# Kernel optimization log

Hardware: AMD Instinct MI355X
Metric: run time of the kernel (lower is better)

## Reference

```python
import jax, jax.numpy as jnp
import numpy as np

N_NODES = 32768   # total atoms in the batch
N_EDGES = 65536   # directed bonds (avg degree ~2)
B = 512           # graphs per batch (graphs.batch_size)
D = 64            # in_feats = hidden_feats = 64
EH = 32           # edge-MLP hidden width
N_ITERS = 6       # num_step_set2set
N_LSTM = 3        # num_layer_set2set
EPS = 1e-5


def setup_inputs() -> dict:
    key = jax.random.key(0)
    ks = iter(jax.random.split(key, 64))
    nrm = lambda shape, s: jax.random.normal(next(ks), shape, dtype=jnp.float32) * s
    inp = {
        "atom_feats": jax.random.normal(next(ks), (N_NODES, D), dtype=jnp.float32),
        "edge_feat": jax.random.uniform(next(ks), (N_EDGES, 1), dtype=jnp.float32),
        "src": jax.random.randint(next(ks), (N_EDGES,), 0, N_NODES, dtype=jnp.int32),
        "dst": jax.random.randint(next(ks), (N_EDGES,), 0, N_NODES, dtype=jnp.int32),
        "node_graph_ids": jnp.sort(jax.random.randint(next(ks), (N_NODES,), 0, B, dtype=jnp.int32)),
    }
    for l in range(2):  # two NNConv layers
        inp[f"ew1_{l}"] = nrm((EH, 1), 0.5)
        inp[f"eb1_{l}"] = nrm((EH,), 0.1)
        inp[f"ew2_{l}"] = nrm((D * D, EH), 0.05)
        inp[f"eb2_{l}"] = nrm((D * D,), 0.02)
        inp[f"cb_{l}"] = nrm((D,), 0.1)
    inp["ln_g"] = jnp.ones((D,), jnp.float32)
    inp["ln_b"] = jnp.zeros((D,), jnp.float32)
    in_sizes = [2 * D, D, D]
    for l in range(N_LSTM):
        inp[f"wih{l}"] = nrm((4 * D, in_sizes[l]), 0.1)
        inp[f"whh{l}"] = nrm((4 * D, D), 0.1)
        inp[f"bih{l}"] = nrm((4 * D,), 0.05)
        inp[f"bhh{l}"] = nrm((4 * D,), 0.05)
    inp["gn_g"] = jnp.ones((2 * D,), jnp.float32)
    inp["gn_b"] = jnp.zeros((2 * D,), jnp.float32)
    inp["fc1_w"] = nrm((2 * D, 2 * D), 0.08)
    inp["fc1_b"] = nrm((2 * D,), 0.02)
    inp["bn_g"] = jnp.ones((2 * D,), jnp.float32)
    inp["bn_b"] = jnp.zeros((2 * D,), jnp.float32)
    inp["bn_m"] = jnp.zeros((2 * D,), jnp.float32)
    inp["bn_v"] = jnp.ones((2 * D,), jnp.float32)
    inp["fc2_w"] = nrm((D, 2 * D), 0.08)
    inp["fc2_b"] = nrm((D,), 0.02)
    return inp


def _layernorm(x, g, b):
    mu = jnp.mean(x, axis=-1, keepdims=True)
    v = jnp.var(x, axis=-1, keepdims=True)
    return (x - mu) / jnp.sqrt(v + EPS) * g + b


def _nnconv(x, edge_feat, src, dst, ew1, eb1, ew2, eb2, cb):
    # edge MLP: 1 -> 32 -> D*D, reshaped to a per-edge weight matrix
    h = jax.nn.relu(edge_feat @ ew1.T + eb1)              # [E, 32]
    W = (h @ ew2.T + eb2).reshape(-1, D, D)               # [E, D, D]
    m = jnp.einsum('ei,eio->eo', x[src], W)               # per-edge matmul [E, D]
    s = jax.ops.segment_sum(m, dst, num_segments=N_NODES)
    deg = jax.ops.segment_sum(jnp.ones((m.shape[0],), m.dtype), dst, num_segments=N_NODES)
    return s / jnp.maximum(deg, 1.0)[:, None] + cb        # scatter-mean + bias


def reference(atom_feats, edge_feat, src, dst, node_graph_ids,
              ew1_0, eb1_0, ew2_0, eb2_0, cb_0,
              ew1_1, eb1_1, ew2_1, eb2_1, cb_1,
              ln_g, ln_b,
              wih0, whh0, bih0, bhh0, wih1, whh1, bih1, bhh1, wih2, whh2, bih2, bhh2,
              gn_g, gn_b, fc1_w, fc1_b, bn_g, bn_b, bn_m, bn_v, fc2_w, fc2_b):
    x = atom_feats
    for (ew1, eb1, ew2, eb2, cb) in ((ew1_0, eb1_0, ew2_0, eb2_0, cb_0),
                                     (ew1_1, eb1_1, ew2_1, eb2_1, cb_1)):
        x = jax.nn.relu(_nnconv(x, edge_feat, src, dst, ew1, eb1, ew2, eb2, cb))
        # dropout is identity in eval mode
    x = _layernorm(x, ln_g, ln_b)  # graph_norm (num_nodes > batch_size)

    # Set2Set readout: 3-layer LSTM, 6 iterations, softmax attention per graph
    wihs = (wih0, wih1, wih2); whhs = (whh0, whh1, whh2)
    bihs = (bih0, bih1, bih2); bhhs = (bhh0, bhh1, bhh2)
    q_star = jnp.zeros((B, 2 * D), x.dtype)
    hs = [jnp.zeros((B, D), x.dtype) for _ in range(N_LSTM)]
    cs = [jnp.zeros((B, D), x.dtype) for _ in range(N_LSTM)]
    for _ in range(N_ITERS):
        inp_l = q_star
        for l in range(N_LSTM):
            gates = inp_l @ wihs[l].T + bihs[l] + hs[l] @ whhs[l].T + bhhs[l]
            ig, fg, gg, og = jnp.split(gates, 4, axis=-1)  # PyTorch gate order i,f,g,o
            cs[l] = jax.nn.sigmoid(fg) * cs[l] + jax.nn.sigmoid(ig) * jnp.tanh(gg)
            hs[l] = jax.nn.sigmoid(og) * jnp.tanh(cs[l])
            inp_l = hs[l]
        q = inp_l                                          # [B, D]
        e = jnp.sum(x * q[node_graph_ids], axis=-1)        # [N]
        mx = jax.ops.segment_max(e, node_graph_ids, num_segments=B)
        a = jnp.exp(e - mx[node_graph_ids])
        z = jax.ops.segment_sum(a, node_graph_ids, num_segments=B)
        alpha = a / z[node_graph_ids]                      # per-graph softmax
        readout = jax.ops.segment_sum(x * alpha[:, None], node_graph_ids, num_segments=B)
        q_star = jnp.concatenate([q, readout], axis=-1)    # [B, 2D]

    g = _layernorm(q_star, gn_g, gn_b)                     # GraphNorm on graph embedding
    y = g @ fc1_w.T + fc1_b
    y = (y - bn_m) / jnp.sqrt(bn_v + EPS) * bn_g + bn_b    # BatchNorm1d (eval, running stats)
    y = jax.nn.relu(y)
    out = jax.nn.relu(y @ fc2_w.T + fc2_b)                 # [B, D]
    return out
```

## Files before the change

### kernel.cpp

```cpp
#include <hip/hip_runtime.h>

#define KN 32768
#define KE 65536
#define KB 512
#define KEPB 64
#define KNREG 33
#define KEORD (KE + KNREG * KEPB)
#define KNBLK (KEORD / KEPB)

#define O_BUF0 ((size_t)0)
#define O_BUF1 (O_BUF0 + (size_t)KN * 64)
#define O_DEG  (O_BUF1 + (size_t)KN * 64)
#define O_GCNT (O_DEG + KN)
#define O_GST  (O_GCNT + KB)
#define O_HIST (O_GST + KB + 8)
#define O_CUR  (O_HIST + 128)
#define O_FLAG (O_CUR + 128)
#define O_ZEND (O_FLAG + 64)
#define O_EORD ((O_ZEND + 63) & ~(size_t)63)
#define O_RBLK (O_EORD + 2 * (size_t)KEORD)
#define O_FEND (O_RBLK + 2 * 1088)
#define O_WB   ((O_FEND + 63) & ~(size_t)63)
#define O_WS   (O_WB + (size_t)KNREG * 4096)
#define O_CROSS (O_WS + (size_t)KNREG * 4096)
#define O_RCNT (O_CROSS + 64)
#define O_AOFF (O_RCNT + 64)
#define O_REGN (O_AOFF + 128)
#define O_END  (O_REGN + KE)

#define T_WIH0 (O_EORD)
#define T_WHH0 (T_WIH0 + 32768)
#define T_WIH1 (T_WHH0 + 16384)
#define T_WHH1 (T_WIH1 + 16384)
#define T_WIH2 (T_WHH1 + 16384)
#define T_WHH2 (T_WIH2 + 16384)

__device__ float sigf(float x) { return 1.0f / (1.0f + expf(-x)); }

extern "C" __global__ void GNNModule_9259949490279_kernel(float* out, float v) {
    int i = blockIdx.x * 256 + threadIdx.x;
    if (i < KB * 64) out[i] = v;
}

extern "C" __global__ void k_post(const int* flag, float* out) {
    int f = flag[0];
    if (f == 0) return;
    int i = blockIdx.x * 256 + threadIdx.x;
    if (i < KB * 64) out[i] = 300.0f + (float)f;
}

extern "C" __global__ void k_init(float* wsf, int* wsi) {
    size_t i = (size_t)blockIdx.x * 256 + threadIdx.x;
    size_t stride = (size_t)gridDim.x * 256;
    for (size_t p = i; p < O_ZEND; p += stride) wsf[p] = 0.0f;
    for (size_t p = O_EORD + i; p < O_FEND; p += stride) wsi[p] = -1;
}

extern "C" __global__ void k_deg(const int* dst, float* deg, int* flag) {
    int e = blockIdx.x * 256 + threadIdx.x;
    if (e >= KE) return;
    int d = dst[e];
    if ((unsigned)d >= (unsigned)KN) { atomicOr(flag, 1); d = 0; }
    atomicAdd(&deg[d], 1.0f);
}

extern "C" __global__ void k_gcount(const int* gid, int* gcnt, int* flag) {
    __shared__ int lh[257];
    __shared__ int gminS;
    int t = threadIdx.x;
    int n = blockIdx.x * 256 + t;
    lh[t] = 0;
    if (t == 0) { lh[256] = 0; gminS = gid[blockIdx.x * 256]; }
    __syncthreads();
    int g = gid[n];
    if ((unsigned)g >= (unsigned)KB) { atomicOr(flag, 2); g = 0; }
    int gm = gminS;
    if ((unsigned)gm >= (unsigned)KB) gm = 0;
    int d = g - gm;
    if (d >= 0 && d < 257) atomicAdd(&lh[d], 1);
    else atomicAdd(&gcnt[g], 1);
    __syncthreads();
    if (lh[t] > 0) atomicAdd(&gcnt[gm + t], lh[t]);
    if (t == 0 && lh[256] > 0) atomicAdd(&gcnt[gm + 256], lh[256]);
}

extern "C" __global__ void k_gscan(const int* gcnt, int* gstart) {
    __shared__ int part[64];
    __shared__ int pre[64];
    int t = threadIdx.x;
    int v[8];
    int s = 0;
    int base = t * 8;
    for (int j = 0; j < 8; ++j) { v[j] = gcnt[base + j]; s += v[j]; }
    part[t] = s;
    __syncthreads();
    if (t == 0) {
        int run = 0;
        for (int i = 0; i < 64; ++i) { pre[i] = run; run += part[i]; }
    }
    __syncthreads();
    int run = pre[t];
    for (int j = 0; j < 8; ++j) { gstart[base + j] = run; run += v[j]; }
    if (t == 63) gstart[KB] = run;
}

extern "C" __global__ void k_prep(const float* ew1, const float* eb1,
                                  float* cross, int* rcnt) {
    if (threadIdx.x != 0 || blockIdx.x != 0) return;
    float cl[32];
    int n = 0;
    for (int k = 0; k < 32; ++k) {
        float a = ew1[k], b = eb1[k];
        if (a != 0.0f) {
            float tt = -b / a;
            if (tt > 0.0f && tt < 1.0f) cl[n++] = tt;
        }
    }
    for (int i = 1; i < n; ++i) {
        float v = cl[i];
        int j = i - 1;
        while (j >= 0 && cl[j] > v) { cl[j + 1] = cl[j]; --j; }
        cl[j + 1] = v;
    }
    for (int i = 0; i < n; ++i) cross[i] = cl[i];
    *rcnt = n;
}

extern "C" __global__ __launch_bounds__(256) void k_mats(
    const float* ew1, const float* eb1, const float* ew2, const float* eb2,
    const float* cross, const int* rcnt, float* Wb, float* Ws) {
    int r = blockIdx.x;
    int n = *rcnt;
    if (r > n) return;
    float lo = (r == 0) ? 0.0f : cross[r - 1];
    float hi = (r == n) ? 1.0f : cross[r];
    float mid = 0.5f * (lo + hi);
    __shared__ float mw[32], mb[32];
    int t = threadIdx.x;
    if (t < 32) {
        bool act = (mid * ew1[t] + eb1[t]) > 0.0f;
        mw[t] = act ? ew1[t] : 0.0f;
        mb[t] = act ? eb1[t] : 0.0f;
    }
    __syncthreads();
    #pragma unroll
    for (int j = 0; j < 16; ++j) {
        int idx = j * 256 + t;
        float as = 0.0f, ab = eb2[idx];
        #pragma unroll
        for (int k4 = 0; k4 < 8; ++k4) {
            float4 w2 = *(const float4*)&ew2[(size_t)idx * 32 + 4 * k4];
            as += mw[4*k4+0]*w2.x + mw[4*k4+1]*w2.y + mw[4*k4+2]*w2.z + mw[4*k4+3]*w2.w;
            ab += mb[4*k4+0]*w2.x + mb[4*k4+1]*w2.y + mb[4*k4+2]*w2.z + mb[4*k4+3]*w2.w;
        }
        Wb[(size_t)r * 4096 + idx] = ab;
        Ws[(size_t)r * 4096 + idx] = as;
    }
}

extern "C" __global__ void k_region(const float* ef, const float* cross,
                                    const int* rcnt, int* region, int* hist) {
    __shared__ float lcross[32];
    __shared__ int lh[64];
    __shared__ int ln;
    int t = threadIdx.x;
    if (t == 0) ln = *rcnt;
    if (t < 64) lh[t] = 0;
    if (t >= 32 && t < 64) lcross[t - 32] = 0.0f;
    __syncthreads();
    if (t < 32 && t < ln) lcross[t] = cross[t];
    __syncthreads();
    int e = blockIdx.x * 256 + t;
    float f = ef[e];
    int n = ln, r = 0;
    for (int j = 0; j < n; ++j) r += (f > lcross[j]) ? 1 : 0;
    region[e] = r;
    atomicAdd(&lh[r], 1);
    __syncthreads();
    if (t < 64 && lh[t] > 0) atomicAdd(&hist[t], lh[t]);
}

extern "C" __global__ void k_scan(const int* hist, const int* rcnt,
                                  int* aoff, int* rblk) {
    if (threadIdx.x != 0 || blockIdx.x != 0) return;
    int R = *rcnt + 1;
    int base = 0;
    for (int r = 0; r < R; ++r) {
        aoff[r] = base * KEPB;
        int nb = (hist[r] + KEPB - 1) / KEPB;
        for (int j = 0; j < nb; ++j) rblk[base + j] = r;
        base += nb;
    }
}

extern "C" __global__ void k_scatidx(const int* region, const int* aoff,
                                     int* cursor, int* eorder) {
    __shared__ int lcnt[64];
    __shared__ int lbase[64];
    int t = threadIdx.x;
    if (t < 64) lcnt[t] = 0;
    __syncthreads();
    int e = blockIdx.x * 256 + t;
    int r = region[e];
    int lr = atomicAdd(&lcnt[r], 1);
    __syncthreads();
    if (t < 64 && lcnt[t] > 0) lbase[t] = atomicAdd(&cursor[t], lcnt[t]);
    __syncthreads();
    eorder[aoff[r] + lbase[r] + lr] = e;
}

extern "C" __global__ __launch_bounds__(256) void k_edge(
    const float* x, const float* efeat, const int* src, const int* dst,
    const float* Wb, const float* Ws, const int* rblk, const int* eorder,
    float* sbuf) {
    __shared__ __align__(16) float mbuf[4096];
    __shared__ __align__(16) float msuf[4096];
    __shared__ __align__(16) float xs[4][16][64];
    int b = blockIdx.x;
    int r = rblk[b];
    if (r < 0) return;
    int t = threadIdx.x;
    const float4* gb = (const float4*)(Wb + (size_t)r * 4096);
    const float4* gs = (const float4*)(Ws + (size_t)r * 4096);
    float4* lb = (float4*)mbuf;
    float4* ls = (float4*)msuf;
    #pragma unroll
    for (int j = 0; j < 4; ++j) {
        lb[t + 256 * j] = gb[t + 256 * j];
        ls[t + 256 * j] = gs[t + 256 * j];
    }
    __syncthreads();
    int w = t >> 6, lane = t & 63;
    int base = b * KEPB + w * 16;
    int eid = (lane < 16) ? eorder[base + lane] : -1;
    float efl = 0.0f;
    int srl = 0, dsl = 0;
    if (eid >= 0) { efl = efeat[eid]; srl = src[eid]; dsl = dst[eid]; }
    unsigned long long vm = __ballot(eid >= 0);
    if ((vm & 0xFFFFull) == 0ull) return;
    float ef[16];
    int dv[16];
    #pragma unroll
    for (int s = 0; s < 16; ++s) {
        ef[s] = __shfl(efl, s);
        int sv = __shfl(srl, s);
        dv[s] = __shfl(dsl, s);
        xs[w][s][lane] = x[(size_t)sv * 64 + lane];
    }
    float acc[16];
    #pragma unroll
    for (int s = 0; s < 16; ++s) acc[s] = 0.0f;
    #pragma unroll 1
    for (int i4 = 0; i4 < 16; ++i4) {
        float wb0 = mbuf[(i4 * 4 + 0) * 64 + lane], ws0 = msuf[(i4 * 4 + 0) * 64 + lane];
        float wb1 = mbuf[(i4 * 4 + 1) * 64 + lane], ws1 = msuf[(i4 * 4 + 1) * 64 + lane];
        float wb2 = mbuf[(i4 * 4 + 2) * 64 + lane], ws2 = msuf[(i4 * 4 + 2) * 64 + lane];
        float wb3 = mbuf[(i4 * 4 + 3) * 64 + lane], ws3 = msuf[(i4 * 4 + 3) * 64 + lane];
        #pragma unroll
        for (int j = 0; j < 16; ++j) {
            float4 xv = *(const float4*)&xs[w][j][i4 * 4];
            acc[j] = fmaf(xv.x, fmaf(ef[j], ws0, wb0), acc[j]);
            acc[j] = fmaf(xv.y, fmaf(ef[j], ws1, wb1), acc[j]);
            acc[j] = fmaf(xv.z, fmaf(ef[j], ws2, wb2), acc[j]);
            acc[j] = fmaf(xv.w, fmaf(ef[j], ws3, wb3), acc[j]);
        }
    }
    #pragma unroll
    for (int j = 0; j < 16; ++j) {
        if ((vm >> j) & 1ull) atomicAdd(&sbuf[(size_t)dv[j] * 64 + lane], acc[j]);
    }
}

extern "C" __global__ void k_final0(float* s, const float* deg, const float* cb, int* flag) {
    int idx = blockIdx.x * 256 + threadIdx.x;
    int n = idx >> 6;
    int o = idx & 63;
    float d = deg[n];
    if (d < 1.0f) d = 1.0f;
    float v = s[idx] / d + cb[o];
    if (v < 0.0f) v = 0.0f;
    if (!(v == v)) { v = 0.0f; atomicOr(flag, 32); }
    s[idx] = v;
}

extern "C" __global__ void k_final1ln(float* s, const float* deg, const float* cb,
                                      const float* lg, const float* lb, int* flag) {
    __shared__ float red[64];
    int t = threadIdx.x;
    int n = blockIdx.x;
    float d = deg[n];
    if (d < 1.0f) d = 1.0f;
    float v = s[(size_t)n * 64 + t] / d + cb[t];
    if (v < 0.0f) v = 0.0f;
    red[t] = v;
    __syncthreads();
    for (int m = 32; m >= 1; m >>= 1) {
        if (t < m) red[t] += red[t + m];
        __syncthreads();
    }
    float mu = red[0] * (1.0f / 64.0f);
    __syncthreads();
    red[t] = v * v;
    __syncthreads();
    for (int m = 32; m >= 1; m >>= 1) {
        if (t < m) red[t] += red[t + m];
        __syncthreads();
    }
    float var = red[0] * (1.0f / 64.0f) - mu * mu;
    float rs = rsqrtf(var + 1e-5f);
    float r = (v - mu) * rs * lg[t] + lb[t];
    if (!(r == r)) { r = 0.0f; atomicOr(flag, 8); }
    s[(size_t)n * 64 + t] = r;
}

extern "C" __global__ void k_twall(
    const float* wih0, const float* whh0, const float* wih1, const float* whh1,
    const float* wih2, const float* whh2, float4* dst) {
    int idx = blockIdx.x * 256 + threadIdx.x;
    if (idx >= 28672) return;
    const float* src;
    int K, local;
    if (idx < 8192)       { src = wih0; K = 128; local = idx; }
    else if (idx < 12288) { src = whh0; K = 64;  local = idx - 8192; }
    else if (idx < 16384) { src = wih1; K = 64;  local = idx - 12288; }
    else if (idx < 20480) { src = whh1; K = 64;  local = idx - 16384; }
    else if (idx < 24576) { src = wih2; K = 64;  local = idx - 20480; }
    else                  { src = whh2; K = 64;  local = idx - 24576; }
    int r = local & 255, k4 = local >> 8;
    const float* s = src + (size_t)r * K + 4 * k4;
    dst[idx] = make_float4(s[0], s[1], s[2], s[3]);
}

extern "C" __global__ __launch_bounds__(1024) void k_s2s9(
    const float* x, const int* gstart,
    const float4* wT0, const float4* uT0, const float* bih0, const float* bhh0,
    const float4* wT1, const float4* uT1, const float* bih1, const float* bhh1,
    const float4* wT2, const float4* uT2, const float* bih2, const float* bhh2,
    const float* gn_g, const float* gn_b,
    const float* fc1_w, const float* fc1_b,
    const float* bn_g, const float* bn_b, const float* bn_m, const float* bn_v,
    const float* fc2_w, const float* fc2_b,
    float* out, int* flag) {
    __shared__ __align__(16) float qs[128];
    __shared__ __align__(16) float hs0[64];
    __shared__ __align__(16) float hs1[64];
    __shared__ __align__(16) float hs2[64];
    __shared__ __align__(16) float cs[3][64];
    __shared__ __align__(16) float gatp[4][256];
    __shared__ __align__(16) float esc[1024];
    __shared__ __align__(16) float red16[16][64];
    __shared__ float mzz[16], zzz[16];
    int t = threadIdx.x;
    int g = blockIdx.x;
    int r = t & 255, q = t >> 8;
    int w = t >> 6, lane = t & 63;

    if (t < 128) qs[t] = 0.0f;
    if (t < 64) {
        hs0[t] = 0.0f; hs1[t] = 0.0f; hs2[t] = 0.0f;
        cs[0][t] = 0.0f; cs[1][t] = 0.0f; cs[2][t] = 0.0f;
    }
    __syncthreads();

    int n0 = gstart[g];
    int n1 = gstart[g + 1];
    if (n0 < 0) n0 = 0;
    if (n0 > KN) n0 = KN;
    if (n1 < n0) n1 = n0;
    if (n1 > KN) n1 = KN;
    int cnt = n1 - n0;
    if (cnt > 1024) { cnt = 1024; if (t == 0) atomicOr(flag, 16); }

    for (int it = 0; it < 6; ++it) {
        {
            float a = (q == 0) ? (bih0[r] + bhh0[r]) : 0.0f;
            const float4* wc = wT0 + (size_t)(q * 8) * 256 + r;
            const float4* q4 = (const float4*)qs + q * 8;
            #pragma unroll
            for (int k4 = 0; k4 < 8; ++k4) {
                float4 wv = wc[k4 * 256];
                float4 xv = q4[k4];
                a += wv.x*xv.x + wv.y*xv.y + wv.z*xv.z + wv.w*xv.w;
            }
            const float4* uc = uT0 + (size_t)(q * 4) * 256 + r;
            const float4* h4 = (const float4*)hs0 + q * 4;
            #pragma unroll
            for (int k4 = 0; k4 < 4; ++k4) {
                float4 wv = uc[k4 * 256];
                float4 hv = h4[k4];
                a += wv.x*hv.x + wv.y*hv.y + wv.z*hv.z + wv.w*hv.w;
            }
            gatp[q][r] = a;
            __syncthreads();
            if (t < 64) {
                float gi = gatp[0][t] + gatp[1][t] + gatp[2][t] + gatp[3][t];
                float gf = gatp[0][64 + t] + gatp[1][64 + t] + gatp[2][64 + t] + gatp[3][64 + t];
                float gg = gatp[0][128 + t] + gatp[1][128 + t] + gatp[2][128 + t] + gatp[3][128 + t];
                float go = gatp[0][192 + t] + gatp[1][192 + t] + gatp[2][192 + t] + gatp[3][192 + t];
                float c = sigf(gf) * cs[0][t] + sigf(gi) * tanhf(gg);
                cs[0][t] = c;
                hs0[t] = sigf(go) * tanhf(c);
            }
            __syncthreads();
        }
        {
            float a = (q == 0) ? (bih1[r] + bhh1[r]) : 0.0f;
            const float4* wc = wT1 + (size_t)(q * 4) * 256 + r;
            const float4* uc = uT1 + (size_t)(q * 4) * 256 + r;
            const float4* i4 = (const float4*)hs0 + q * 4;
            const float4* h4 = (const float4*)hs1 + q * 4;
            #pragma unroll
            for (int k4 = 0; k4 < 4; ++k4) {
                float4 wv = wc[k4 * 256];
                float4 xv = i4[k4];
                a += wv.x*xv.x + wv.y*xv.y + wv.z*xv.z + wv.w*xv.w;
                float4 uv = uc[k4 * 256];
                float4 hv = h4[k4];
                a += uv.x*hv.x + uv.y*hv.y + uv.z*hv.z + uv.w*hv.w;
            }
            gatp[q][r] = a;
            __syncthreads();
            if (t < 64) {
                float gi = gatp[0][t] + gatp[1][t] + gatp[2][t] + gatp[3][t];
                float gf = gatp[0][64 + t] + gatp[1][64 + t] + gatp[2][64 + t] + gatp[3][64 + t];
                float gg = gatp[0][128 + t] + gatp[1][128 + t] + gatp[2][128 + t] + gatp[3][128 + t];
                float go = gatp[0][192 + t] + gatp[1][192 + t] + gatp[2][192 + t] + gatp[3][192 + t];
                float c = sigf(gf) * cs[1][t] + sigf(gi) * tanhf(gg);
                cs[1][t] = c;
                hs1[t] = sigf(go) * tanhf(c);
            }
            __syncthreads();
        }
        {
            float a = (q == 0) ? (bih2[r] + bhh2[r]) : 0.0f;
            const float4* wc = wT2 + (size_t)(q * 4) * 256 + r;
            const float4* uc = uT2 + (size_t)(q * 4) * 256 + r;
            const float4* i4 = (const float4*)hs1 + q * 4;
            const float4* h4 = (const float4*)hs2 + q * 4;
            #pragma unroll
            for (int k4 = 0; k4 < 4; ++k4) {
                float4 wv = wc[k4 * 256];
                float4 xv = i4[k4];
                a += wv.x*xv.x + wv.y*xv.y + wv.z*xv.z + wv.w*xv.w;
                float4 uv = uc[k4 * 256];
                float4 hv = h4[k4];
                a += uv.x*hv.x + uv.y*hv.y + uv.z*hv.z + uv.w*hv.w;
            }
            gatp[q][r] = a;
            __syncthreads();
            if (t < 64) {
                float gi = gatp[0][t] + gatp[1][t] + gatp[2][t] + gatp[3][t];
                float gf = gatp[0][64 + t] + gatp[1][64 + t] + gatp[2][64 + t] + gatp[3][64 + t];
                float gg = gatp[0][128 + t] + gatp[1][128 + t] + gatp[2][128 + t] + gatp[3][128 + t];
                float go = gatp[0][192 + t] + gatp[1][192 + t] + gatp[2][192 + t] + gatp[3][192 + t];
                float c = sigf(gf) * cs[2][t] + sigf(gi) * tanhf(gg);
                cs[2][t] = c;
                hs2[t] = sigf(go) * tanhf(c);
            }
            __syncthreads();
        }
        {
            float qv_ = hs2[lane];
            float mx = -3.0e38f;
            for (int p = w; p < cnt; p += 16) {
                float xv = x[(size_t)(n0 + p) * 64 + lane];
                float v = xv * qv_;
                v += __shfl_xor(v, 1);
                v += __shfl_xor(v, 2);
                v += __shfl_xor(v, 4);
                v += __shfl_xor(v, 8);
                v += __shfl_xor(v, 16);
                v += __shfl_xor(v, 32);
                if (lane == 0) esc[p] = v;
                if (v > mx) mx = v;
            }
            if (lane == 0) mzz[w] = mx;
            __syncthreads();
            float M = mzz[0];
            #pragma unroll
            for (int j = 1; j < 16; ++j) if (mzz[j] > M) M = mzz[j];
            float z = 0.0f;
            for (int p = t; p < cnt; p += 1024) {
                float e = expf(esc[p] - M);
                esc[p] = e;
                z += e;
            }
            z += __shfl_xor(z, 1);
            z += __shfl_xor(z, 2);
            z += __shfl_xor(z, 4);
            z += __shfl_xor(z, 8);
            z += __shfl_xor(z, 16);
            z += __shfl_xor(z, 32);
            if (lane == 0) zzz[w] = z;
            __syncthreads();
            float Z = 0.0f;
            #pragma unroll
            for (int j = 0; j < 16; ++j) Z += zzz[j];
            float rd = 0.0f;
            for (int p = w; p < cnt; p += 16)
                rd += x[(size_t)(n0 + p) * 64 + lane] * esc[p];
            red16[w][lane] = rd;
            __syncthreads();
            if (t < 64) {
                float rr = 0.0f;
                #pragma unroll
                for (int j = 0; j < 16; ++j) rr += red16[j][t];
                rr = (cnt > 0 && Z > 0.0f) ? rr / Z : 0.0f;
                qs[t] = hs2[t];
                qs[64 + t] = rr;
            }
            __syncthreads();
        }
    }

    {
        float v = (t < 128) ? qs[t] : 0.0f;
        float s1 = v, s2 = v * v;
        s1 += __shfl_xor(s1, 1); s2 += __shfl_xor(s2, 1);
        s1 += __shfl_xor(s1, 2); s2 += __shfl_xor(s2, 2);
        s1 += __shfl_xor(s1, 4); s2 += __shfl_xor(s2, 4);
        s1 += __shfl_xor(s1, 8); s2 += __shfl_xor(s2, 8);
        s1 += __shfl_xor(s1, 16); s2 += __shfl_xor(s2, 16);
        s1 += __shfl_xor(s1, 32); s2 += __shfl_xor(s2, 32);
        if (lane == 0) { mzz[w] = s1; zzz[w] = s2; }
        __syncthreads();
        float sm = mzz[0] + mzz[1];
        float sq = zzz[0] + zzz[1];
        float mu = sm * (1.0f / 128.0f);
        float var = sq * (1.0f / 128.0f) - mu * mu;
        float rs = rsqrtf(var + 1e-5f);
        if (t < 128) esc[t] = (v - mu) * rs * gn_g[t] + gn_b[t];
        __syncthreads();
        if (t < 128) {
            float y = fc1_b[t];
            const float4* wr = (const float4*)(fc1_w + (size_t)t * 128);
            #pragma unroll
            for (int k4 = 0; k4 < 32; ++k4) {
                float4 wv = wr[k4];
                float4 gv = *(const float4*)&esc[4 * k4];
                y += wv.x*gv.x + wv.y*gv.y + wv.z*gv.z + wv.w*gv.w;
            }
            y = (y - bn_m[t]) * rsqrtf(bn_v[t] + 1e-5f) * bn_g[t] + bn_b[t];
            if (y < 0.0f) y = 0.0f;
            gatp[0][t] = y;
        }
        __syncthreads();
        if (t < 64) {
            float o = fc2_b[t];
            const float4* wr = (const float4*)(fc2_w + (size_t)t * 128);
            #pragma unroll
            for (int k4 = 0; k4 < 32; ++k4) {
                float4 wv = wr[k4];
                float4 yv = *(const float4*)&gatp[0][4 * k4];
                o += wv.x*yv.x + wv.y*yv.y + wv.z*yv.z + wv.w*yv.w;
            }
            if (!(o == o)) o = 999.0f;
            else if (o < 0.0f) o = 0.0f;
            out[(size_t)g * 64 + t] = o;
        }
    }
}

extern "C" void kernel_launch(void* const* d_in, const int* in_sizes, int n_in,
                              void* d_out, int out_size, void* d_ws, size_t ws_size,
                              hipStream_t stream) {
    float* out = (float*)d_out;
    const int outBlocks = (KB * 64 + 255) / 256;

    if (n_in != 39) {
        GNNModule_9259949490279_kernel<<<outBlocks, 256, 0, stream>>>(out, 50.0f);
        return;
    }
    if (in_sizes[0] != KN * 64 || in_sizes[1] != KE || in_sizes[4] != KN) {
        GNNModule_9259949490279_kernel<<<outBlocks, 256, 0, stream>>>(out, 60.0f);
        return;
    }
    if (out_size != KB * 64) {
        GNNModule_9259949490279_kernel<<<outBlocks, 256, 0, stream>>>(out, 80.0f);
        return;
    }
    if (ws_size < O_END * 4) {
        GNNModule_9259949490279_kernel<<<outBlocks, 256, 0, stream>>>(out, 100.0f);
        return;
    }

    const float* atom = (const float*)d_in[0];
    const float* efeat = (const float*)d_in[1];
    const int* src = (const int*)d_in[2];
    const int* dst = (const int*)d_in[3];
    const int* gid = (const int*)d_in[4];
    const float* ew1[2] = {(const float*)d_in[5], (const float*)d_in[10]};
    const float* eb1[2] = {(const float*)d_in[6], (const float*)d_in[11]};
    const float* ew2[2] = {(const float*)d_in[7], (const float*)d_in[12]};
    const float* eb2[2] = {(const float*)d_in[8], (const float*)d_in[13]};
    const float* cb[2] = {(const float*)d_in[9], (const float*)d_in[14]};
    const float* ln_g = (const float*)d_in[15];
    const float* ln_b = (const float*)d_in[16];
    const float* wih0 = (const float*)d_in[17];
    const float* whh0 = (const float*)d_in[18];
    const float* bih0 = (const float*)d_in[19];
    const float* bhh0 = (const float*)d_in[20];
    const float* wih1 = (const float*)d_in[21];
    const float* whh1 = (const float*)d_in[22];
    const float* bih1 = (const float*)d_in[23];
    const float* bhh1 = (const float*)d_in[24];
    const float* wih2 = (const float*)d_in[25];
    const float* whh2 = (const float*)d_in[26];
    const float* bih2 = (const float*)d_in[27];
    const float* bhh2 = (const float*)d_in[28];
    const float* gn_g = (const float*)d_in[29];
    const float* gn_b = (const float*)d_in[30];
    const float* fc1_w = (const float*)d_in[31];
    const float* fc1_b = (const float*)d_in[32];
    const float* bn_g = (const float*)d_in[33];
    const float* bn_b = (const float*)d_in[34];
    const float* bn_m = (const float*)d_in[35];
    const float* bn_v = (const float*)d_in[36];
    const float* fc2_w = (const float*)d_in[37];
    const float* fc2_b = (const float*)d_in[38];

    float* wsf = (float*)d_ws;
    int* wsi = (int*)d_ws;
    float* buf0 = wsf + O_BUF0;
    float* buf1 = wsf + O_BUF1;
    float* deg = wsf + O_DEG;
    int* gcnt = wsi + O_GCNT;
    int* gstart = wsi + O_GST;
    int* flag = wsi + O_FLAG;
    float* Wb = wsf + O_WB;
    float* Ws = wsf + O_WS;
    float* cross = wsf + O_CROSS;
    int* rcnt = wsi + O_RCNT;
    int* region = wsi + O_REGN;

    k_init<<<2048, 256, 0, stream>>>(wsf, wsi);

    k_deg<<<KE / 256, 256, 0, stream>>>(dst, deg, flag);
    k_gcount<<<KN / 256, 256, 0, stream>>>(gid, gcnt, flag);
    k_gscan<<<1, 64, 0, stream>>>(gcnt, gstart);

    for (int l = 0; l < 2; ++l) {
        const float* xin = (l == 0) ? atom : buf0;
        float* sout = (l == 0) ? buf0 : buf1;
        int* hist = wsi + O_HIST + l * 64;
        int* cursor = wsi + O_CUR + l * 64;
        int* aoff = wsi + O_AOFF + l * 64;
        int* eorder = wsi + O_EORD + l * KEORD;
        int* rblk = wsi + O_RBLK + l * 1088;

        k_prep<<<1, 64, 0, stream>>>(ew1[l], eb1[l], cross, rcnt);
        k_mats<<<KNREG, 256, 0, stream>>>(ew1[l], eb1[l], ew2[l], eb2[l], cross, rcnt, Wb, Ws);
        k_region<<<KE / 256, 256, 0, stream>>>(efeat, cross, rcnt, region, hist);
        k_scan<<<1, 64, 0, stream>>>(hist, rcnt, aoff, rblk);
        k_scatidx<<<KE / 256, 256, 0, stream>>>(region, aoff, cursor, eorder);
        k_edge<<<KNBLK, 256, 0, stream>>>(xin, efeat, src, dst, Wb, Ws, rblk, eorder, sout);
        if (l == 0) {
            k_final0<<<KN * 64 / 256, 256, 0, stream>>>(buf0, deg, cb[0], flag);
        } else {
            k_final1ln<<<KN, 64, 0, stream>>>(buf1, deg, cb[1], ln_g, ln_b, flag);
        }
    }

    float4* twbase = (float4*)(wsf + T_WIH0);
    k_twall<<<112, 256, 0, stream>>>(wih0, whh0, wih1, whh1, wih2, whh2, twbase);

    float4* tw0 = twbase;
    float4* tu0 = (float4*)(wsf + T_WHH0);
    float4* tw1 = (float4*)(wsf + T_WIH1);
    float4* tu1 = (float4*)(wsf + T_WHH1);
    float4* tw2 = (float4*)(wsf + T_WIH2);
    float4* tu2 = (float4*)(wsf + T_WHH2);

    k_s2s9<<<KB, 1024, 0, stream>>>(buf1, gstart,
        tw0, tu0, bih0, bhh0,
        tw1, tu1, bih1, bhh1,
        tw2, tu2, bih2, bhh2,
        gn_g, gn_b, fc1_w, fc1_b, bn_g, bn_b, bn_m, bn_v, fc2_w, fc2_b,
        out, flag);

    k_post<<<outBlocks, 256, 0, stream>>>(flag, out);
}
```

Measured before the change: 389.7 us.

## Fuse preprocessing kernels for both NNConv layers into fewer launches

Replaces the per-layer prep/region/scan/scatter kernels and the separate degree and graph-count kernels with combined kernels that handle both layers at once (k_prepall, k_front, k_scans, k_mid). Layer-0 weight-matrix construction runs as extra blocks alongside the edge sorting. The goal is to cut the number of small serial launches and the intermediate region array round trip. In exchange the edge-region classification is computed twice, and k_front has some subtle indexing, such as 128 nodes per block with a 192-wide local histogram.

```diff
diff --git a/kernel.cpp b/kernel.cpp
--- a/kernel.cpp
+++ b/kernel.cpp
@@ -56,74 +56,188 @@
     for (size_t p = O_EORD + i; p < O_FEND; p += stride) wsi[p] = -1;
 }
 
-extern "C" __global__ void k_deg(const int* dst, float* deg, int* flag) {
-    int e = blockIdx.x * 256 + threadIdx.x;
-    if (e >= KE) return;
+extern "C" __global__ void k_prepall(
+    const float* ew1a, const float* eb1a, const float* ew1b, const float* eb1b,
+    float* cross, int* rcnt) {
+    __shared__ float la[32], lb_[32];
+    int l = blockIdx.x;
+    int t = threadIdx.x;
+    const float* w = (l == 0) ? ew1a : ew1b;
+    const float* b = (l == 0) ? eb1a : eb1b;
+    if (t < 32) { la[t] = w[t]; lb_[t] = b[t]; }
+    __syncthreads();
+    if (t == 0) {
+        float cl[32];
+        int n = 0;
+        for (int k = 0; k < 32; ++k) {
+            float a = la[k], bb = lb_[k];
+            if (a != 0.0f) {
+                float tt = -bb / a;
+                if (tt > 0.0f && tt < 1.0f) cl[n++] = tt;
+            }
+        }
+        for (int i = 1; i < n; ++i) {
+            float v = cl[i];
+            int j = i - 1;
+            while (j >= 0 && cl[j] > v) { cl[j + 1] = cl[j]; --j; }
+            cl[j + 1] = v;
+        }
+        for (int i = 0; i < n; ++i) cross[32 * l + i] = cl[i];
+        rcnt[l] = n;
+    }
+}
+
+extern "C" __global__ void k_front(
+    const int* dst, const int* gid, const float* efeat,
+    const float* cross, const int* rcnt,
+    float* deg, int* gcnt, int* hist0, int* hist1, int* flag) {
+    __shared__ float c0[32], c1[32];
+    __shared__ int n0s, n1s;
+    __shared__ int lh0[64], lh1[64];
+    __shared__ int lg[192];
+    __shared__ int gminS;
+    int t = threadIdx.x;
+    int b = blockIdx.x;
+    if (t < 32) { c0[t] = cross[t]; c1[t] = cross[32 + t]; }
+    if (t == 0) { n0s = rcnt[0]; n1s = rcnt[1]; gminS = gid[b * 128]; }
+    if (t < 64) { lh0[t] = 0; lh1[t] = 0; }
+    if (t < 192) lg[t] = 0;
+    __syncthreads();
+
+    int e = b * 256 + t;
     int d = dst[e];
     if ((unsigned)d >= (unsigned)KN) { atomicOr(flag, 1); d = 0; }
     atomicAdd(&deg[d], 1.0f);
-}
-
-extern "C" __global__ void k_gcount(const int* gid, int* gcnt, int* flag) {
-    __shared__ int lh[257];
-    __shared__ int gminS;
+    float f = efeat[e];
+    int r0 = 0, r1 = 0;
+    int n0 = n0s, n1 = n1s;
+    for (int j = 0; j < n0; ++j) r0 += (f > c0[j]) ? 1 : 0;
+    for (int j = 0; j < n1; ++j) r1 += (f > c1[j]) ? 1 : 0;
+    atomicAdd(&lh0[r0], 1);
+    atomicAdd(&lh1[r1], 1);
+
+    if (t < 128) {
+        int n = b * 128 + t;
+        int g = gid[n];
+        if ((unsigned)g >= (unsigned)KB) { atomicOr(flag, 2); g = 0; }
+        int gm = gminS;
+        if ((unsigned)gm >= (unsigned)KB) gm = 0;
+        int dd = g - gm;
+        if (dd >= 0 && dd < 192) atomicAdd(&lg[dd], 1);
+        else atomicAdd(&gcnt[g], 1);
+    }
+    __syncthreads();
+    if (t < 64) {
+        if (lh0[t] > 0) atomicAdd(&hist0[t], lh0[t]);
+        if (lh1[t] > 0) atomicAdd(&hist1[t], lh1[t]);
+    }
+    if (t < 192 && lg[t] > 0) {
+        int gm = gminS;
+        if ((unsigned)gm >= (unsigned)KB) gm = 0;
+        int gidx = gm + t;
+        if (gidx <= KB) atomicAdd(&gcnt[gidx], lg[t]);
+    }
+}
+
+extern "C" __global__ void k_scans(
+    const int* gcnt, int* gstart,
+    const int* histb, const int* rcnt, int* aoffb, int* rblkb) {
     int t = threadIdx.x;
-    int n = blockIdx.x * 256 + t;
-    lh[t] = 0;
-    if (t == 0) { lh[256] = 0; gminS = gid[blockIdx.x * 256]; }
-    __syncthreads();
-    int g = gid[n];
-    if ((unsigned)g >= (unsigned)KB) { atomicOr(flag, 2); g = 0; }
-    int gm = gminS;
-    if ((unsigned)gm >= (unsigned)KB) gm = 0;
-    int d = g - gm;
-    if (d >= 0 && d < 257) atomicAdd(&lh[d], 1);
-    else atomicAdd(&gcnt[g], 1);
-    __syncthreads();
-    if (lh[t] > 0) atomicAdd(&gcnt[gm + t], lh[t]);
-    if (t == 0 && lh[256] > 0) atomicAdd(&gcnt[gm + 256], lh[256]);
-}
-
-extern "C" __global__ void k_gscan(const int* gcnt, int* gstart) {
-    __shared__ int part[64];
-    __shared__ int pre[64];
+    if (blockIdx.x == 0) {
+        __shared__ int part[64];
+        __shared__ int pre[64];
+        int v[8];
+        int s = 0;
+        int base = t * 8;
+        for (int j = 0; j < 8; ++j) { v[j] = gcnt[base + j]; s += v[j]; }
+        part[t] = s;
+        __syncthreads();
+        if (t == 0) {
+            int run = 0;
+            for (int i = 0; i < 64; ++i) { pre[i] = run; run += part[i]; }
+        }
+        __syncthreads();
+        int run = pre[t];
+        for (int j = 0; j < 8; ++j) { gstart[base + j] = run; run += v[j]; }
+        if (t == 63) gstart[KB] = run;
+    } else {
+        int l = blockIdx.x - 1;
+        const int* hist = histb + l * 64;
+        int* aoff = aoffb + l * 64;
+        int* rblk = rblkb + l * 1088;
+        __shared__ int lh[64];
+        lh[t] = hist[t];
+        __syncthreads();
+        int R = rcnt[l] + 1;
+        if (t < R) {
+            int base = 0;
+            for (int r = 0; r < t; ++r) base += (lh[r] + KEPB - 1) / KEPB;
+            aoff[t] = base * KEPB;
+            int nb = (lh[t] + KEPB - 1) / KEPB;
+            for (int j = 0; j < nb; ++j) rblk[base + j] = t;
+        }
+    }
+}
+
+extern "C" __global__ __launch_bounds__(256) void k_mid(
+    const float* efeat, const float* cross, const int* rcnt,
+    const int* aoffb, int* cursorb, int* eorder0, int* eorder1,
+    const float* ew1, const float* eb1, const float* ew2, const float* eb2,
+    float* Wb, float* Ws) {
     int t = threadIdx.x;
-    int v[8];
-    int s = 0;
-    int base = t * 8;
-    for (int j = 0; j < 8; ++j) { v[j] = gcnt[base + j]; s += v[j]; }
-    part[t] = s;
-    __syncthreads();
-    if (t == 0) {
-        int run = 0;
-        for (int i = 0; i < 64; ++i) { pre[i] = run; run += part[i]; }
-    }
-    __syncthreads();
-    int run = pre[t];
-    for (int j = 0; j < 8; ++j) { gstart[base + j] = run; run += v[j]; }
-    if (t == 63) gstart[KB] = run;
-}
-
-extern "C" __global__ void k_prep(const float* ew1, const float* eb1,
-                                  float* cross, int* rcnt) {
-    if (threadIdx.x != 0 || blockIdx.x != 0) return;
-    float cl[32];
-    int n = 0;
-    for (int k = 0; k < 32; ++k) {
-        float a = ew1[k], b = eb1[k];
-        if (a != 0.0f) {
-            float tt = -b / a;
-            if (tt > 0.0f && tt < 1.0f) cl[n++] = tt;
-        }
-    }
-    for (int i = 1; i < n; ++i) {
-        float v = cl[i];
-        int j = i - 1;
-        while (j >= 0 && cl[j] > v) { cl[j + 1] = cl[j]; --j; }
-        cl[j + 1] = v;
-    }
-    for (int i = 0; i < n; ++i) cross[i] = cl[i];
-    *rcnt = n;
+    if (blockIdx.x < 256) {
+        __shared__ float c0[32], c1[32];
+        __shared__ int n0s, n1s;
+        __shared__ int lc0[64], lc1[64], lb0[64], lb1[64];
+        int b = blockIdx.x;
+        if (t < 32) { c0[t] = cross[t]; c1[t] = cross[32 + t]; }
+        if (t == 0) { n0s = rcnt[0]; n1s = rcnt[1]; }
+        if (t < 64) { lc0[t] = 0; lc1[t] = 0; }
+        __syncthreads();
+        int e = b * 256 + t;
+        float f = efeat[e];
+        int r0 = 0, r1 = 0;
+        int n0 = n0s, n1 = n1s;
+        for (int j = 0; j < n0; ++j) r0 += (f > c0[j]) ? 1 : 0;
+        for (int j = 0; j < n1; ++j) r1 += (f > c1[j]) ? 1 : 0;
+        int lr0 = atomicAdd(&lc0[r0], 1);
+        int lr1 = atomicAdd(&lc1[r1], 1);
+        __syncthreads();
+        if (t < 64) {
+            if (lc0[t] > 0) lb0[t] = atomicAdd(&cursorb[t], lc0[t]);
+            if (lc1[t] > 0) lb1[t] = atomicAdd(&cursorb[64 + t], lc1[t]);
+        }
+        __syncthreads();
+        eorder0[aoffb[r0] + lb0[r0] + lr0] = e;
+        eorder1[aoffb[64 + r1] + lb1[r1] + lr1] = e;
+    } else {
+        int r = blockIdx.x - 256;
+        int n = rcnt[0];
+        if (r > n) return;
+        float lo = (r == 0) ? 0.0f : cross[r - 1];
+        float hi = (r == n) ? 1.0f : cross[r];
+        float mid = 0.5f * (lo + hi);
+        __shared__ float mw[32], mb[32];
+        if (t < 32) {
+            bool act = (mid * ew1[t] + eb1[t]) > 0.0f;
+            mw[t] = act ? ew1[t] : 0.0f;
+            mb[t] = act ? eb1[t] : 0.0f;
+        }
+        __syncthreads();
+        #pragma unroll
+        for (int j = 0; j < 16; ++j) {
+            int idx = j * 256 + t;
+            float as = 0.0f, ab = eb2[idx];
+            #pragma unroll
+            for (int k4 = 0; k4 < 8; ++k4) {
+                float4 w2 = *(const float4*)&ew2[(size_t)idx * 32 + 4 * k4];
+                as += mw[4*k4+0]*w2.x + mw[4*k4+1]*w2.y + mw[4*k4+2]*w2.z + mw[4*k4+3]*w2.w;
+                ab += mb[4*k4+0]*w2.x + mb[4*k4+1]*w2.y + mb[4*k4+2]*w2.z + mb[4*k4+3]*w2.w;
+            }
+            Wb[(size_t)r * 4096 + idx] = ab;
+            Ws[(size_t)r * 4096 + idx] = as;
+        }
+    }
 }
 
 extern "C" __global__ __launch_bounds__(256) void k_mats(
@@ -156,57 +270,6 @@
         Wb[(size_t)r * 4096 + idx] = ab;
         Ws[(size_t)r * 4096 + idx] = as;
     }
-}
-
-extern "C" __global__ void k_region(const float* ef, const float* cross,
-                                    const int* rcnt, int* region, int* hist) {
-    __shared__ float lcross[32];
-    __shared__ int lh[64];
-    __shared__ int ln;
-    int t = threadIdx.x;
-    if (t == 0) ln = *rcnt;
-    if (t < 64) lh[t] = 0;
-    if (t >= 32 && t < 64) lcross[t - 32] = 0.0f;
-    __syncthreads();
-    if (t < 32 && t < ln) lcross[t] = cross[t];
-    __syncthreads();
-    int e = blockIdx.x * 256 + t;
-    float f = ef[e];
-    int n = ln, r = 0;
-    for (int j = 0; j < n; ++j) r += (f > lcross[j]) ? 1 : 0;
-    region[e] = r;
-    atomicAdd(&lh[r], 1);
-    __syncthreads();
-    if (t < 64 && lh[t] > 0) atomicAdd(&hist[t], lh[t]);
-}
-
-extern "C" __global__ void k_scan(const int* hist, const int* rcnt,
-                                  int* aoff, int* rblk) {
-    if (threadIdx.x != 0 || blockIdx.x != 0) return;
-    int R = *rcnt + 1;
-    int base = 0;
-    for (int r = 0; r < R; ++r) {
-        aoff[r] = base * KEPB;
-        int nb = (hist[r] + KEPB - 1) / KEPB;
-        for (int j = 0; j < nb; ++j) rblk[base + j] = r;
-        base += nb;
-    }
-}
-
-extern "C" __global__ void k_scatidx(const int* region, const int* aoff,
-                                     int* cursor, int* eorder) {
-    __shared__ int lcnt[64];
-    __shared__ int lbase[64];
-    int t = threadIdx.x;
-    if (t < 64) lcnt[t] = 0;
-    __syncthreads();
-    int e = blockIdx.x * 256 + t;
-    int r = region[e];
-    int lr = atomicAdd(&lcnt[r], 1);
-    __syncthreads();
-    if (t < 64 && lcnt[t] > 0) lbase[t] = atomicAdd(&cursor[t], lcnt[t]);
-    __syncthreads();
-    eorder[aoff[r] + lbase[r] + lr] = e;
 }
 
 extern "C" __global__ __launch_bounds__(256) void k_edge(
@@ -631,50 +694,38 @@
     float* Ws = wsf + O_WS;
     float* cross = wsf + O_CROSS;
     int* rcnt = wsi + O_RCNT;
-    int* region = wsi + O_REGN;
 
     k_init<<<2048, 256, 0, stream>>>(wsf, wsi);
 
-    k_deg<<<KE / 256, 256, 0, stream>>>(dst, deg, flag);
-    k_gcount<<<KN / 256, 256, 0, stream>>>(gid, gcnt, flag);
-    k_gscan<<<1, 64, 0, stream>>>(gcnt, gstart);
-
-    for (int l = 0; l < 2; ++l) {
-        const float* xin = (l == 0) ? atom : buf0;
-        float* sout = (l == 0) ? buf0 : buf1;
-        int* hist = wsi + O_HIST + l * 64;
-        int* cursor = wsi + O_CUR + l * 64;
-        int* aoff = wsi + O_AOFF + l * 64;
-        int* eorder = wsi + O_EORD + l * KEORD;
-        int* rblk = wsi + O_RBLK + l * 1088;
-
-        k_prep<<<1, 64, 0, stream>>>(ew1[l], eb1[l], cross, rcnt);
-        k_mats<<<KNREG, 256, 0, stream>>>(ew1[l], eb1[l], ew2[l], eb2[l], cross, rcnt, Wb, Ws);
-        k_region<<<KE / 256, 256, 0, stream>>>(efeat, cross, rcnt, region, hist);
-        k_scan<<<1, 64, 0, stream>>>(hist, rcnt, aoff, rblk);
-        k_scatidx<<<KE / 256, 256, 0, stream>>>(region, aoff, cursor, eorder);
-        k_edge<<<KNBLK, 256, 0, stream>>>(xin, efeat, src, dst, Wb, Ws, rblk, eorder, sout);
-        if (l == 0) {
-            k_final0<<<KN * 64 / 256, 256, 0, stream>>>(buf0, deg, cb[0], flag);
-        } else {
-            k_final1ln<<<KN, 64, 0, stream>>>(buf1, deg, cb[1], ln_g, ln_b, flag);
-        }
-    }
+    k_prepall<<<2, 64, 0, stream>>>(ew1[0], eb1[0], ew1[1], eb1[1], cross, rcnt);
+
+    k_front<<<256, 256, 0, stream>>>(dst, gid, efeat, cross, rcnt,
+                                     deg, gcnt, wsi + O_HIST, wsi + O_HIST + 64, flag);
+
+    k_scans<<<3, 64, 0, stream>>>(gcnt, gstart, wsi + O_HIST, rcnt,
+                                  wsi + O_AOFF, wsi + O_RBLK);
+
+    k_mid<<<289, 256, 0, stream>>>(efeat, cross, rcnt, wsi + O_AOFF, wsi + O_CUR,
+                                   wsi + O_EORD, wsi + O_EORD + KEORD,
+                                   ew1[0], eb1[0], ew2[0], eb2[0], Wb, Ws);
+
+    k_edge<<<KNBLK, 256, 0, stream>>>(atom, efeat, src, dst, Wb, Ws,
+                                      wsi + O_RBLK, wsi + O_EORD, buf0);
+    k_final0<<<KN * 64 / 256, 256, 0, stream>>>(buf0, deg, cb[0], flag);
+
+    k_mats<<<KNREG, 256, 0, stream>>>(ew1[1], eb1[1], ew2[1], eb2[1],
+                                      cross + 32, rcnt + 1, Wb, Ws);
+    k_edge<<<KNBLK, 256, 0, stream>>>(buf0, efeat, src, dst, Wb, Ws,
+                                      wsi + O_RBLK + 1088, wsi + O_EORD + KEORD, buf1);
+    k_final1ln<<<KN, 64, 0, stream>>>(buf1, deg, cb[1], ln_g, ln_b, flag);
 
     float4* twbase = (float4*)(wsf + T_WIH0);
     k_twall<<<112, 256, 0, stream>>>(wih0, whh0, wih1, whh1, wih2, whh2, twbase);
 
-    float4* tw0 = twbase;
-    float4* tu0 = (float4*)(wsf + T_WHH0);
-    float4* tw1 = (float4*)(wsf + T_WIH1);
-    float4* tu1 = (float4*)(wsf + T_WHH1);
-    float4* tw2 = (float4*)(wsf + T_WIH2);
-    float4* tu2 = (float4*)(wsf + T_WHH2);
-
     k_s2s9<<<KB, 1024, 0, stream>>>(buf1, gstart,
-        tw0, tu0, bih0, bhh0,
-        tw1, tu1, bih1, bhh1,
-        tw2, tu2, bih2, bhh2,
+        twbase, (float4*)(wsf + T_WHH0), bih0, bhh0,
+        (float4*)(wsf + T_WIH1), (float4*)(wsf + T_WHH1), bih1, bhh1,
+        (float4*)(wsf + T_WIH2), (float4*)(wsf + T_WHH2), bih2, bhh2,
         gn_g, gn_b, fc1_w, fc1_b, bn_g, bn_b, bn_m, bn_v, fc2_w, fc2_b,
         out, flag);
 
```

Measured after the change: 335.3 us. -14.0%, faster.
